# Kernel optimization log

Measured on AMD Instinct MI355X. Metric: run time of the kernel, lower is better.

## Reference

```python
import jax, jax.numpy as jnp
import numpy as np

N, D, P, R, T, K = 200000, 128, 4096, 4, 3, 16

def setup_inputs() -> dict:
    key = jax.random.key(0)
    ks = jax.random.split(key, 9)
    return {
        "node_embeds": jax.random.normal(ks[0], (N, D), jnp.float32),
        "node_pairs": jax.random.randint(ks[1], (P, 2), 0, N),
        "node_type_ids": jax.random.randint(ks[2], (N,), 0, T),
        "neighbor_idx": jax.random.randint(ks[3], (P, 2, R, K), 0, N),
        "delta_t": jax.random.uniform(ks[4], (P, 2, R, K), jnp.float32),
        "W_phi": jax.random.normal(ks[5], (T, D, D), jnp.float32) * 0.05,
        "W_zeta": jax.random.normal(ks[6], (2 * D,), jnp.float32) * 0.05,
        "W_beta_w": jax.random.normal(ks[7], (R, D, D), jnp.float32) * 0.05,
        "W_beta_b": jax.random.normal(ks[8], (R, D), jnp.float32) * 0.05,
    }

def reference(node_embeds, node_pairs, node_type_ids, neighbor_idx, delta_t,
              W_phi, W_zeta, W_beta_w, W_beta_b):
    n = node_embeds.shape[0]
    # per-node type-specific linear: compute all types then select (T small)
    H_all = jnp.einsum('nd,tde->tne', node_embeds, W_phi)        # [T,N,D]
    H = H_all[node_type_ids, jnp.arange(n)]                      # [N,D]
    # micro attention: e = W_zeta([h_n; h_s]) * exp(-dt), softmax over K neighbors
    zn, zs = W_zeta[:D], W_zeta[D:]
    h_n = H[neighbor_idx]                                        # [P,2,R,K,D]
    e_n = jnp.einsum('psrkd,d->psrk', h_n, zn)
    e_s = jnp.einsum('psd,d->ps', H[node_pairs], zs)             # [P,2]
    e = (e_n + e_s[:, :, None, None]) * jnp.exp(-delta_t)        # [P,2,R,K]
    alpha = jax.nn.softmax(e, axis=-1)
    # meso: attention-weighted aggregation per relation, then per-relation linear
    h_nei = node_embeds[neighbor_idx]                            # [P,2,R,K,D]
    h_agg = jnp.einsum('psrk,psrkd->psrd', alpha, h_nei)         # [P,2,R,D]
    h_beta = jnp.einsum('psrd,rde->psre', h_agg, W_beta_w) + W_beta_b
    # macro: average over both pair sides and relations, sigmoid combine
    x_tilde = h_beta.mean(axis=(1, 2))                           # [P,D]
    return jax.nn.sigmoid(x_tilde)
```

## Files before the change

### kernel.cpp

```cpp
#include <hip/hip_runtime.h>
#include <hip/hip_bf16.h>

#define NN 200000
#define D 128
#define P 4096
#define R 4
#define T 3
#define K 16

__device__ __forceinline__ float bf2f(unsigned int u) {
    union { unsigned int i; float f; } c;
    c.i = u << 16;
    return c.f;
}
__device__ __forceinline__ unsigned short f2bf(float x) {
    union { float f; unsigned int i; } c; c.f = x;
    unsigned int r = c.i + 0x7FFFu + ((c.i >> 16) & 1u);
    return (unsigned short)(r >> 16);
}
__device__ __forceinline__ float ldE(const void* p, size_t i, int f32) {
    return f32 ? ((const float*)p)[i] : bf2f(((const unsigned short*)p)[i]);
}
__device__ __forceinline__ void ld8(const void* p, size_t off, int f32, float* o) {
    if (f32) {
        const float* q = (const float*)p + off;
        float4 a = *(const float4*)q;
        float4 b = *(const float4*)(q + 4);
        o[0]=a.x; o[1]=a.y; o[2]=a.z; o[3]=a.w;
        o[4]=b.x; o[5]=b.y; o[6]=b.z; o[7]=b.w;
    } else {
        uint4 r = *(const uint4*)((const unsigned short*)p + off);
        o[0]=bf2f(r.x & 0xffffu); o[1]=bf2f(r.x >> 16);
        o[2]=bf2f(r.y & 0xffffu); o[3]=bf2f(r.y >> 16);
        o[4]=bf2f(r.z & 0xffffu); o[5]=bf2f(r.z >> 16);
        o[6]=bf2f(r.w & 0xffffu); o[7]=bf2f(r.w >> 16);
    }
}

__global__ void detect_dtype(const unsigned short* __restrict__ emb, int* __restrict__ flag) {
    int tid = threadIdx.x;
    int bad = 0;
    #pragma unroll
    for (int i = 0; i < 4; ++i) {
        unsigned short u = emb[(size_t)(tid * 4 + i) * 2 * 97];
        unsigned int e = (u >> 7) & 0xFFu;
        if (e >= 147u) bad = 1;
    }
    int any_bad = __any(bad);
    if (tid == 0) *flag = any_bad ? 1 : 0;
}

__global__ void precompute_vu(const void* __restrict__ W_phi,
                              const void* __restrict__ W_zeta,
                              const int* __restrict__ flag,
                              float* __restrict__ ws_v, float* __restrict__ ws_u) {
    const int f32 = *flag;
    const int t = blockIdx.x;
    const int d = threadIdx.x;
    const size_t rb = (size_t)(t * D + d) * D;
    float av = 0.f, au = 0.f;
    for (int e = 0; e < D; e += 8) {
        float w[8], zn[8], zs[8];
        ld8(W_phi, rb + e, f32, w);
        ld8(W_zeta, e, f32, zn);
        ld8(W_zeta, D + e, f32, zs);
        #pragma unroll
        for (int q = 0; q < 8; ++q) { av += w[q] * zn[q]; au += w[q] * zs[q]; }
    }
    ws_v[t * D + d] = av;
    ws_u[t * D + d] = au;
}

__global__ __launch_bounds__(256) void precompute_c(
    const void* __restrict__ emb, const int* __restrict__ types,
    const float* __restrict__ ws_v, const float* __restrict__ ws_u,
    const int* __restrict__ flag,
    float* __restrict__ c, float* __restrict__ c2)
{
    __shared__ float vsh[T * D], ush[T * D];
    const int f32 = *flag;
    const int tid = threadIdx.x;
    for (int i = tid; i < T * D; i += 256) { vsh[i] = ws_v[i]; ush[i] = ws_u[i]; }
    __syncthreads();
    const int w = tid >> 6, l = tid & 63;
    const int grp = l >> 4, ch = l & 15;
    const int nbase = blockIdx.x * 64 + w * 4 + grp;

    int   tt[4];
    float rv[4][8];
    #pragma unroll
    for (int it = 0; it < 4; ++it) {
        int n = nbase + it * 16;
        tt[it] = types[n];
        ld8(emb, (size_t)n * D + ch * 8, f32, rv[it]);
    }
    #pragma unroll
    for (int it = 0; it < 4; ++it) {
        int n = nbase + it * 16;
        const float* vp = vsh + tt[it] * D + ch * 8;
        const float* up = ush + tt[it] * D + ch * 8;
        float a = 0.f, b = 0.f;
        #pragma unroll
        for (int q = 0; q < 8; ++q) { a += rv[it][q] * vp[q]; b += rv[it][q] * up[q]; }
        #pragma unroll
        for (int off = 1; off <= 8; off <<= 1) {
            a += __shfl_xor(a, off, 64);
            b += __shfl_xor(b, off, 64);
        }
        if (ch == 0) { c[n] = a; c2[n] = b; }
    }
}

__global__ __launch_bounds__(256, 4) void fused_kernel(
    const void* __restrict__ emb,
    const int* __restrict__ pairs,
    const int* __restrict__ nbr,
    const void* __restrict__ dlt,
    const void* __restrict__ W_beta_w,
    const void* __restrict__ W_beta_b,
    const float* __restrict__ c,
    const float* __restrict__ c2,
    const int* __restrict__ flag,
    void* __restrict__ out)
{
    const int f32  = *flag;
    const int tid  = threadIdx.x;
    const int wv   = tid >> 6;
    const int l    = tid & 63;
    const int p    = blockIdx.x * 4 + wv;
    const int rsub = l >> 4;
    const int ch   = l & 15;
    const int base = p * 2 * R * K;

    int nb0 = nbr[base + l];
    int nb1 = nbr[base + 64 + l];
    float cs0 = c2[pairs[p * 2]];
    float cs1 = c2[pairs[p * 2 + 1]];
    float dt0 = ldE(dlt, (size_t)base + l, f32);
    float dt1 = ldE(dlt, (size_t)base + 64 + l, f32);
    float e0 = (c[nb0] + cs0) * __expf(-dt0);
    float e1 = (c[nb1] + cs1) * __expf(-dt1);

    float m0 = e0, m1 = e1;
    #pragma unroll
    for (int off = 1; off <= 8; off <<= 1) {
        m0 = fmaxf(m0, __shfl_xor(m0, off, 64));
        m1 = fmaxf(m1, __shfl_xor(m1, off, 64));
    }
    float a0 = __expf(e0 - m0), a1 = __expf(e1 - m1);
    float s0 = a0, s1 = a1;
    #pragma unroll
    for (int off = 1; off <= 8; off <<= 1) {
        s0 += __shfl_xor(s0, off, 64);
        s1 += __shfl_xor(s1, off, 64);
    }
    a0 *= (1.f / s0);
    a1 *= (1.f / s1);

    float y[8] = {0.f,0.f,0.f,0.f,0.f,0.f,0.f,0.f};
    const unsigned short* eu = (const unsigned short*)emb;
    const unsigned short* Wu = (const unsigned short*)W_beta_w;

    #pragma unroll
    for (int r = 0; r < R; ++r) {
        float acc[8] = {0.f,0.f,0.f,0.f,0.f,0.f,0.f,0.f};
        if (!f32) {
            uint4 rbv[8]; float av[8];
            #pragma unroll
            for (int i = 0; i < 8; ++i) {
                int srcl = r * 16 + (i & 3) * 4 + rsub;
                int nb   = __shfl((i >> 2) ? nb1 : nb0, srcl, 64);
                av[i]    = __shfl((i >> 2) ? a1  : a0,  srcl, 64);
                rbv[i]   = *(const uint4*)(eu + (size_t)nb * D + ch * 8);
            }
            #pragma unroll
            for (int i = 0; i < 8; ++i) {
                float a = av[i];
                acc[0] += a * bf2f(rbv[i].x & 0xffffu); acc[1] += a * bf2f(rbv[i].x >> 16);
                acc[2] += a * bf2f(rbv[i].y & 0xffffu); acc[3] += a * bf2f(rbv[i].y >> 16);
                acc[4] += a * bf2f(rbv[i].z & 0xffffu); acc[5] += a * bf2f(rbv[i].z >> 16);
                acc[6] += a * bf2f(rbv[i].w & 0xffffu); acc[7] += a * bf2f(rbv[i].w >> 16);
            }
        } else {
            #pragma unroll
            for (int i = 0; i < 8; ++i) {
                int srcl = r * 16 + (i & 3) * 4 + rsub;
                int nb   = __shfl((i >> 2) ? nb1 : nb0, srcl, 64);
                float a  = __shfl((i >> 2) ? a1  : a0,  srcl, 64);
                float rv[8]; ld8(emb, (size_t)nb * D + ch * 8, 1, rv);
                #pragma unroll
                for (int q = 0; q < 8; ++q) acc[q] += a * rv[q];
            }
        }
        #pragma unroll
        for (int q = 0; q < 8; ++q) {
            acc[q] += __shfl_xor(acc[q], 16, 64);
            acc[q] += __shfl_xor(acc[q], 32, 64);
        }
        #pragma unroll
        for (int dd = 0; dd < 32; ++dd) {
            float gd = __shfl(acc[dd & 7], ((l & 48) >> 2) + (dd >> 3), 64);
            size_t wo = ((size_t)(r * D + (rsub * 32 + dd))) * D + ch * 8;
            if (!f32) {
                uint4 wr = *(const uint4*)(Wu + wo);
                y[0] += gd * bf2f(wr.x & 0xffffu); y[1] += gd * bf2f(wr.x >> 16);
                y[2] += gd * bf2f(wr.y & 0xffffu); y[3] += gd * bf2f(wr.y >> 16);
                y[4] += gd * bf2f(wr.z & 0xffffu); y[5] += gd * bf2f(wr.z >> 16);
                y[6] += gd * bf2f(wr.w & 0xffffu); y[7] += gd * bf2f(wr.w >> 16);
            } else {
                float wb[8]; ld8(W_beta_w, wo, 1, wb);
                #pragma unroll
                for (int q = 0; q < 8; ++q) y[q] += gd * wb[q];
            }
        }
    }

    #pragma unroll
    for (int q = 0; q < 8; ++q) {
        y[q] += __shfl_xor(y[q], 16, 64);
        y[q] += __shfl_xor(y[q], 32, 64);
    }

    float bs[8] = {0.f,0.f,0.f,0.f,0.f,0.f,0.f,0.f};
    #pragma unroll
    for (int r = 0; r < R; ++r) {
        float bb[8]; ld8(W_beta_b, (size_t)r * D + ch * 8, f32, bb);
        #pragma unroll
        for (int q = 0; q < 8; ++q) bs[q] += bb[q];
    }
    if (rsub == 0) {
        float o[8];
        #pragma unroll
        for (int q = 0; q < 8; ++q) {
            float x = (y[q] + 2.f * bs[q]) * 0.125f;
            o[q] = 1.f / (1.f + __expf(-x));
        }
        size_t ob = (size_t)p * D + ch * 8;
        if (f32) {
            *(float4*)((float*)out + ob)     = make_float4(o[0], o[1], o[2], o[3]);
            *(float4*)((float*)out + ob + 4) = make_float4(o[4], o[5], o[6], o[7]);
        } else {
            uint4 pk;
            pk.x = (unsigned int)f2bf(o[0]) | ((unsigned int)f2bf(o[1]) << 16);
            pk.y = (unsigned int)f2bf(o[2]) | ((unsigned int)f2bf(o[3]) << 16);
            pk.z = (unsigned int)f2bf(o[4]) | ((unsigned int)f2bf(o[5]) << 16);
            pk.w = (unsigned int)f2bf(o[6]) | ((unsigned int)f2bf(o[7]) << 16);
            *(uint4*)((unsigned short*)out + ob) = pk;
        }
    }
}

extern "C" void kernel_launch(void* const* d_in, const int* in_sizes, int n_in,
                              void* d_out, int out_size, void* d_ws, size_t ws_size,
                              hipStream_t stream) {
    const void* emb    = d_in[0];
    const int*  pairs  = (const int*)d_in[1];
    const int*  types  = (const int*)d_in[2];
    const int*  nbr    = (const int*)d_in[3];
    const void* dlt    = d_in[4];
    const void* W_phi  = d_in[5];
    const void* W_zeta = d_in[6];
    const void* W_bw   = d_in[7];
    const void* W_bb   = d_in[8];

    int*   flag = (int*)d_ws;
    float* ws_v = (float*)d_ws + 64;
    float* ws_u = ws_v + T * D;
    float* c    = (float*)d_ws + 1024;
    float* c2   = c + NN;

    detect_dtype<<<dim3(1), dim3(64), 0, stream>>>((const unsigned short*)emb, flag);
    precompute_vu<<<dim3(T), dim3(D), 0, stream>>>(W_phi, W_zeta, flag, ws_v, ws_u);
    precompute_c<<<dim3(NN / 64), dim3(256), 0, stream>>>(emb, types, ws_v, ws_u, flag, c, c2);
    fused_kernel<<<dim3(P / 4), dim3(256), 0, stream>>>(emb, pairs, nbr, dlt,
                                                        W_bw, W_bb, c, c2, flag, d_out);
}
```

Measured before the change: 294.4 us.

## Compute attention logits on gathered rows only and split beta projection into GEMM kernel

Drops the precompute pass that computed per-node logit scalars for all 200k nodes. The gather kernel now computes the logits only for the gathered neighbor and pair rows, reusing the embedding rows it already loads for aggregation. The per-relation aggregate is written to a bf16 workspace, and a separate kernel applies W_beta over 16 pairs per block, reading the aggregates from shared memory. This avoids streaming the whole embedding table but adds an intermediate round-trip and rounds the aggregate to bf16 even on the f32 path, which costs precision.

```diff
diff --git a/kernel.cpp b/kernel.cpp
--- a/kernel.cpp
+++ b/kernel.cpp
@@ -71,58 +71,19 @@
     ws_u[t * D + d] = au;
 }
 
-__global__ __launch_bounds__(256) void precompute_c(
-    const void* __restrict__ emb, const int* __restrict__ types,
-    const float* __restrict__ ws_v, const float* __restrict__ ws_u,
-    const int* __restrict__ flag,
-    float* __restrict__ c, float* __restrict__ c2)
-{
-    __shared__ float vsh[T * D], ush[T * D];
-    const int f32 = *flag;
-    const int tid = threadIdx.x;
-    for (int i = tid; i < T * D; i += 256) { vsh[i] = ws_v[i]; ush[i] = ws_u[i]; }
-    __syncthreads();
-    const int w = tid >> 6, l = tid & 63;
-    const int grp = l >> 4, ch = l & 15;
-    const int nbase = blockIdx.x * 64 + w * 4 + grp;
-
-    int   tt[4];
-    float rv[4][8];
-    #pragma unroll
-    for (int it = 0; it < 4; ++it) {
-        int n = nbase + it * 16;
-        tt[it] = types[n];
-        ld8(emb, (size_t)n * D + ch * 8, f32, rv[it]);
-    }
-    #pragma unroll
-    for (int it = 0; it < 4; ++it) {
-        int n = nbase + it * 16;
-        const float* vp = vsh + tt[it] * D + ch * 8;
-        const float* up = ush + tt[it] * D + ch * 8;
-        float a = 0.f, b = 0.f;
-        #pragma unroll
-        for (int q = 0; q < 8; ++q) { a += rv[it][q] * vp[q]; b += rv[it][q] * up[q]; }
-        #pragma unroll
-        for (int off = 1; off <= 8; off <<= 1) {
-            a += __shfl_xor(a, off, 64);
-            b += __shfl_xor(b, off, 64);
-        }
-        if (ch == 0) { c[n] = a; c2[n] = b; }
-    }
-}
-
-__global__ __launch_bounds__(256, 4) void fused_kernel(
+__global__ __launch_bounds__(256, 2) void gather_kernel(
     const void* __restrict__ emb,
     const int* __restrict__ pairs,
+    const int* __restrict__ types,
     const int* __restrict__ nbr,
     const void* __restrict__ dlt,
-    const void* __restrict__ W_beta_w,
-    const void* __restrict__ W_beta_b,
-    const float* __restrict__ c,
-    const float* __restrict__ c2,
+    const float* __restrict__ ws_v,
+    const float* __restrict__ ws_u,
     const int* __restrict__ flag,
-    void* __restrict__ out)
+    unsigned short* __restrict__ g)
 {
+    __shared__ __align__(16) float vsh[T * D];
+    __shared__ __align__(16) float ush[T * D];
     const int f32  = *flag;
     const int tid  = threadIdx.x;
     const int wv   = tid >> 6;
@@ -132,50 +93,90 @@
     const int ch   = l & 15;
     const int base = p * 2 * R * K;
 
+    for (int i = tid; i < T * D; i += 256) { vsh[i] = ws_v[i]; ush[i] = ws_u[i]; }
+    __syncthreads();
+
     int nb0 = nbr[base + l];
     int nb1 = nbr[base + 64 + l];
-    float cs0 = c2[pairs[p * 2]];
-    float cs1 = c2[pairs[p * 2 + 1]];
     float dt0 = ldE(dlt, (size_t)base + l, f32);
     float dt1 = ldE(dlt, (size_t)base + 64 + l, f32);
-    float e0 = (c[nb0] + cs0) * __expf(-dt0);
-    float e1 = (c[nb1] + cs1) * __expf(-dt1);
-
-    float m0 = e0, m1 = e1;
-    #pragma unroll
-    for (int off = 1; off <= 8; off <<= 1) {
-        m0 = fmaxf(m0, __shfl_xor(m0, off, 64));
-        m1 = fmaxf(m1, __shfl_xor(m1, off, 64));
-    }
-    float a0 = __expf(e0 - m0), a1 = __expf(e1 - m1);
-    float s0 = a0, s1 = a1;
-    #pragma unroll
-    for (int off = 1; off <= 8; off <<= 1) {
-        s0 += __shfl_xor(s0, off, 64);
-        s1 += __shfl_xor(s1, off, 64);
-    }
-    a0 *= (1.f / s0);
-    a1 *= (1.f / s1);
-
-    float y[8] = {0.f,0.f,0.f,0.f,0.f,0.f,0.f,0.f};
+    int t0 = types[nb0];
+    int t1 = types[nb1];
+
+    float es01 = 0.f;
+    if (l < 32) {
+        int s  = rsub;
+        int ns = pairs[p * 2 + s];
+        int ts = types[ns];
+        float rv[8]; ld8(emb, (size_t)ns * D + ch * 8, f32, rv);
+        const float* up = ush + ts * D + ch * 8;
+        float a = 0.f;
+        #pragma unroll
+        for (int q = 0; q < 8; ++q) a += rv[q] * up[q];
+        #pragma unroll
+        for (int off = 1; off <= 8; off <<= 1) a += __shfl_xor(a, off, 64);
+        es01 = a;
+    }
+    float es0 = __shfl(es01, 0, 64);
+    float es1 = __shfl(es01, 16, 64);
+
     const unsigned short* eu = (const unsigned short*)emb;
-    const unsigned short* Wu = (const unsigned short*)W_beta_w;
-
-    #pragma unroll
+
     for (int r = 0; r < R; ++r) {
+        int snb[8]; float sdt[8]; int stp[8];
+        #pragma unroll
+        for (int i = 0; i < 8; ++i) {
+            int srcl = r * 16 + (i & 3) * 4 + rsub;
+            snb[i] = __shfl((i >> 2) ? nb1 : nb0, srcl, 64);
+            sdt[i] = __shfl((i >> 2) ? dt1 : dt0, srcl, 64);
+            stp[i] = __shfl((i >> 2) ? t1  : t0,  srcl, 64);
+        }
+
+        float en[8];
         float acc[8] = {0.f,0.f,0.f,0.f,0.f,0.f,0.f,0.f};
+
         if (!f32) {
-            uint4 rbv[8]; float av[8];
+            uint4 rbv[8];
+            #pragma unroll
+            for (int i = 0; i < 8; ++i)
+                rbv[i] = *(const uint4*)(eu + (size_t)snb[i] * D + ch * 8);
             #pragma unroll
             for (int i = 0; i < 8; ++i) {
-                int srcl = r * 16 + (i & 3) * 4 + rsub;
-                int nb   = __shfl((i >> 2) ? nb1 : nb0, srcl, 64);
-                av[i]    = __shfl((i >> 2) ? a1  : a0,  srcl, 64);
-                rbv[i]   = *(const uint4*)(eu + (size_t)nb * D + ch * 8);
+                const float* vp = vsh + stp[i] * D + ch * 8;
+                float4 v0 = *(const float4*)vp;
+                float4 v1 = *(const float4*)(vp + 4);
+                float a = 0.f;
+                a += bf2f(rbv[i].x & 0xffffu) * v0.x + bf2f(rbv[i].x >> 16) * v0.y;
+                a += bf2f(rbv[i].y & 0xffffu) * v0.z + bf2f(rbv[i].y >> 16) * v0.w;
+                a += bf2f(rbv[i].z & 0xffffu) * v1.x + bf2f(rbv[i].z >> 16) * v1.y;
+                a += bf2f(rbv[i].w & 0xffffu) * v1.z + bf2f(rbv[i].w >> 16) * v1.w;
+                #pragma unroll
+                for (int off = 1; off <= 8; off <<= 1) a += __shfl_xor(a, off, 64);
+                en[i] = a;
             }
+            float ef[8];
+            #pragma unroll
+            for (int i = 0; i < 8; ++i)
+                ef[i] = (en[i] + ((i >> 2) ? es1 : es0)) * __expf(-sdt[i]);
+            float m0 = fmaxf(fmaxf(ef[0], ef[1]), fmaxf(ef[2], ef[3]));
+            float m1 = fmaxf(fmaxf(ef[4], ef[5]), fmaxf(ef[6], ef[7]));
+            m0 = fmaxf(m0, __shfl_xor(m0, 16, 64)); m0 = fmaxf(m0, __shfl_xor(m0, 32, 64));
+            m1 = fmaxf(m1, __shfl_xor(m1, 16, 64)); m1 = fmaxf(m1, __shfl_xor(m1, 32, 64));
+            float al[8], s0 = 0.f, s1 = 0.f;
+            #pragma unroll
+            for (int i = 0; i < 4; ++i) { al[i] = __expf(ef[i] - m0); s0 += al[i]; }
+            #pragma unroll
+            for (int i = 4; i < 8; ++i) { al[i] = __expf(ef[i] - m1); s1 += al[i]; }
+            s0 += __shfl_xor(s0, 16, 64); s0 += __shfl_xor(s0, 32, 64);
+            s1 += __shfl_xor(s1, 16, 64); s1 += __shfl_xor(s1, 32, 64);
+            float i0 = 1.f / s0, i1 = 1.f / s1;
+            #pragma unroll
+            for (int i = 0; i < 4; ++i) al[i] *= i0;
+            #pragma unroll
+            for (int i = 4; i < 8; ++i) al[i] *= i1;
             #pragma unroll
             for (int i = 0; i < 8; ++i) {
-                float a = av[i];
+                float a = al[i];
                 acc[0] += a * bf2f(rbv[i].x & 0xffffu); acc[1] += a * bf2f(rbv[i].x >> 16);
                 acc[2] += a * bf2f(rbv[i].y & 0xffffu); acc[3] += a * bf2f(rbv[i].y >> 16);
                 acc[4] += a * bf2f(rbv[i].z & 0xffffu); acc[5] += a * bf2f(rbv[i].z >> 16);
@@ -184,69 +185,129 @@
         } else {
             #pragma unroll
             for (int i = 0; i < 8; ++i) {
-                int srcl = r * 16 + (i & 3) * 4 + rsub;
-                int nb   = __shfl((i >> 2) ? nb1 : nb0, srcl, 64);
-                float a  = __shfl((i >> 2) ? a1  : a0,  srcl, 64);
-                float rv[8]; ld8(emb, (size_t)nb * D + ch * 8, 1, rv);
+                float rv[8]; ld8(emb, (size_t)snb[i] * D + ch * 8, 1, rv);
+                const float* vp = vsh + stp[i] * D + ch * 8;
+                float a = 0.f;
                 #pragma unroll
-                for (int q = 0; q < 8; ++q) acc[q] += a * rv[q];
+                for (int q = 0; q < 8; ++q) a += rv[q] * vp[q];
+                #pragma unroll
+                for (int off = 1; off <= 8; off <<= 1) a += __shfl_xor(a, off, 64);
+                en[i] = a;
             }
-        }
+            float ef[8];
+            #pragma unroll
+            for (int i = 0; i < 8; ++i)
+                ef[i] = (en[i] + ((i >> 2) ? es1 : es0)) * __expf(-sdt[i]);
+            float m0 = fmaxf(fmaxf(ef[0], ef[1]), fmaxf(ef[2], ef[3]));
+            float m1 = fmaxf(fmaxf(ef[4], ef[5]), fmaxf(ef[6], ef[7]));
+            m0 = fmaxf(m0, __shfl_xor(m0, 16, 64)); m0 = fmaxf(m0, __shfl_xor(m0, 32, 64));
+            m1 = fmaxf(m1, __shfl_xor(m1, 16, 64)); m1 = fmaxf(m1, __shfl_xor(m1, 32, 64));
+            float al[8], s0 = 0.f, s1 = 0.f;
+            #pragma unroll
+            for (int i = 0; i < 4; ++i) { al[i] = __expf(ef[i] - m0); s0 += al[i]; }
+            #pragma unroll
+            for (int i = 4; i < 8; ++i) { al[i] = __expf(ef[i] - m1); s1 += al[i]; }
+            s0 += __shfl_xor(s0, 16, 64); s0 += __shfl_xor(s0, 32, 64);
+            s1 += __shfl_xor(s1, 16, 64); s1 += __shfl_xor(s1, 32, 64);
+            float i0 = 1.f / s0, i1 = 1.f / s1;
+            #pragma unroll
+            for (int i = 0; i < 4; ++i) al[i] *= i0;
+            #pragma unroll
+            for (int i = 4; i < 8; ++i) al[i] *= i1;
+            #pragma unroll
+            for (int i = 0; i < 8; ++i) {
+                float rv[8]; ld8(emb, (size_t)snb[i] * D + ch * 8, 1, rv);
+                #pragma unroll
+                for (int q = 0; q < 8; ++q) acc[q] += al[i] * rv[q];
+            }
+        }
+
         #pragma unroll
         for (int q = 0; q < 8; ++q) {
             acc[q] += __shfl_xor(acc[q], 16, 64);
             acc[q] += __shfl_xor(acc[q], 32, 64);
         }
-        #pragma unroll
-        for (int dd = 0; dd < 32; ++dd) {
-            float gd = __shfl(acc[dd & 7], ((l & 48) >> 2) + (dd >> 3), 64);
-            size_t wo = ((size_t)(r * D + (rsub * 32 + dd))) * D + ch * 8;
-            if (!f32) {
-                uint4 wr = *(const uint4*)(Wu + wo);
-                y[0] += gd * bf2f(wr.x & 0xffffu); y[1] += gd * bf2f(wr.x >> 16);
-                y[2] += gd * bf2f(wr.y & 0xffffu); y[3] += gd * bf2f(wr.y >> 16);
-                y[4] += gd * bf2f(wr.z & 0xffffu); y[5] += gd * bf2f(wr.z >> 16);
-                y[6] += gd * bf2f(wr.w & 0xffffu); y[7] += gd * bf2f(wr.w >> 16);
-            } else {
-                float wb[8]; ld8(W_beta_w, wo, 1, wb);
-                #pragma unroll
-                for (int q = 0; q < 8; ++q) y[q] += gd * wb[q];
-            }
-        }
-    }
-
-    #pragma unroll
-    for (int q = 0; q < 8; ++q) {
-        y[q] += __shfl_xor(y[q], 16, 64);
-        y[q] += __shfl_xor(y[q], 32, 64);
+        if (rsub == 0) {
+            uint4 pk;
+            pk.x = (unsigned int)f2bf(acc[0]) | ((unsigned int)f2bf(acc[1]) << 16);
+            pk.y = (unsigned int)f2bf(acc[2]) | ((unsigned int)f2bf(acc[3]) << 16);
+            pk.z = (unsigned int)f2bf(acc[4]) | ((unsigned int)f2bf(acc[5]) << 16);
+            pk.w = (unsigned int)f2bf(acc[6]) | ((unsigned int)f2bf(acc[7]) << 16);
+            *(uint4*)(g + ((size_t)p * R + r) * D + ch * 8) = pk;
+        }
+    }
+}
+
+__global__ __launch_bounds__(256, 2) void beta_gemm(
+    const unsigned short* __restrict__ g,
+    const void* __restrict__ W_bw,
+    const void* __restrict__ W_bb,
+    const int* __restrict__ flag,
+    void* __restrict__ out)
+{
+    __shared__ float gl[16 * 513];
+    const int f32 = *flag;
+    const int tid = threadIdx.x;
+    const int pl  = tid >> 4;
+    const int eb  = (tid & 15) * 8;
+    const size_t pbase = (size_t)blockIdx.x * 16 * 512;
+
+    for (int i = tid * 8; i < 16 * 512; i += 256 * 8) {
+        float v[8]; ld8(g, pbase + i, 0, v);
+        int pp = i >> 9, kk = i & 511;
+        #pragma unroll
+        for (int q = 0; q < 8; ++q) gl[pp * 513 + kk + q] = v[q];
+    }
+    __syncthreads();
+
+    float y[8] = {0.f,0.f,0.f,0.f,0.f,0.f,0.f,0.f};
+    const unsigned short* Wu = (const unsigned short*)W_bw;
+    if (!f32) {
+        #pragma unroll 8
+        for (int k = 0; k < 512; ++k) {
+            float gd = gl[pl * 513 + k];
+            uint4 wr = *(const uint4*)(Wu + (size_t)k * D + eb);
+            y[0] += gd * bf2f(wr.x & 0xffffu); y[1] += gd * bf2f(wr.x >> 16);
+            y[2] += gd * bf2f(wr.y & 0xffffu); y[3] += gd * bf2f(wr.y >> 16);
+            y[4] += gd * bf2f(wr.z & 0xffffu); y[5] += gd * bf2f(wr.z >> 16);
+            y[6] += gd * bf2f(wr.w & 0xffffu); y[7] += gd * bf2f(wr.w >> 16);
+        }
+    } else {
+        #pragma unroll 4
+        for (int k = 0; k < 512; ++k) {
+            float gd = gl[pl * 513 + k];
+            float wb[8]; ld8(W_bw, (size_t)k * D + eb, 1, wb);
+            #pragma unroll
+            for (int q = 0; q < 8; ++q) y[q] += gd * wb[q];
+        }
     }
 
     float bs[8] = {0.f,0.f,0.f,0.f,0.f,0.f,0.f,0.f};
     #pragma unroll
     for (int r = 0; r < R; ++r) {
-        float bb[8]; ld8(W_beta_b, (size_t)r * D + ch * 8, f32, bb);
+        float bb[8]; ld8(W_bb, (size_t)r * D + eb, f32, bb);
         #pragma unroll
         for (int q = 0; q < 8; ++q) bs[q] += bb[q];
     }
-    if (rsub == 0) {
-        float o[8];
-        #pragma unroll
-        for (int q = 0; q < 8; ++q) {
-            float x = (y[q] + 2.f * bs[q]) * 0.125f;
-            o[q] = 1.f / (1.f + __expf(-x));
-        }
-        size_t ob = (size_t)p * D + ch * 8;
-        if (f32) {
-            *(float4*)((float*)out + ob)     = make_float4(o[0], o[1], o[2], o[3]);
-            *(float4*)((float*)out + ob + 4) = make_float4(o[4], o[5], o[6], o[7]);
-        } else {
-            uint4 pk;
-            pk.x = (unsigned int)f2bf(o[0]) | ((unsigned int)f2bf(o[1]) << 16);
-            pk.y = (unsigned int)f2bf(o[2]) | ((unsigned int)f2bf(o[3]) << 16);
-            pk.z = (unsigned int)f2bf(o[4]) | ((unsigned int)f2bf(o[5]) << 16);
-            pk.w = (unsigned int)f2bf(o[6]) | ((unsigned int)f2bf(o[7]) << 16);
-            *(uint4*)((unsigned short*)out + ob) = pk;
-        }
+
+    int p = blockIdx.x * 16 + pl;
+    size_t ob = (size_t)p * D + eb;
+    float o[8];
+    #pragma unroll
+    for (int q = 0; q < 8; ++q) {
+        float x = (y[q] + 2.f * bs[q]) * 0.125f;
+        o[q] = 1.f / (1.f + __expf(-x));
+    }
+    if (f32) {
+        *(float4*)((float*)out + ob)     = make_float4(o[0], o[1], o[2], o[3]);
+        *(float4*)((float*)out + ob + 4) = make_float4(o[4], o[5], o[6], o[7]);
+    } else {
+        uint4 pk;
+        pk.x = (unsigned int)f2bf(o[0]) | ((unsigned int)f2bf(o[1]) << 16);
+        pk.y = (unsigned int)f2bf(o[2]) | ((unsigned int)f2bf(o[3]) << 16);
+        pk.z = (unsigned int)f2bf(o[4]) | ((unsigned int)f2bf(o[5]) << 16);
+        pk.w = (unsigned int)f2bf(o[6]) | ((unsigned int)f2bf(o[7]) << 16);
+        *(uint4*)((unsigned short*)out + ob) = pk;
     }
 }
 
@@ -266,12 +327,11 @@
     int*   flag = (int*)d_ws;
     float* ws_v = (float*)d_ws + 64;
     float* ws_u = ws_v + T * D;
-    float* c    = (float*)d_ws + 1024;
-    float* c2   = c + NN;
+    unsigned short* g = (unsigned short*)((float*)d_ws + 1024);
 
     detect_dtype<<<dim3(1), dim3(64), 0, stream>>>((const unsigned short*)emb, flag);
     precompute_vu<<<dim3(T), dim3(D), 0, stream>>>(W_phi, W_zeta, flag, ws_v, ws_u);
-    precompute_c<<<dim3(NN / 64), dim3(256), 0, stream>>>(emb, types, ws_v, ws_u, flag, c, c2);
-    fused_kernel<<<dim3(P / 4), dim3(256), 0, stream>>>(emb, pairs, nbr, dlt,
-                                                        W_bw, W_bb, c, c2, flag, d_out);
-}
+    gather_kernel<<<dim3(P / 4), dim3(256), 0, stream>>>(emb, pairs, types, nbr, dlt,
+                                                         ws_v, ws_u, flag, g);
+    beta_gemm<<<dim3(P / 16), dim3(256), 0, stream>>>(g, W_bw, W_bb, flag, d_out);
+}
```

Result: faster. 283.2 us (-3.8%).

## Compute attention scores on gathered neighbors instead of precomputing per-node table

Applied to the files above, without the earlier changes.

Drops the precompute_c pass over all 200k nodes. The neighbor attention logits are now computed inside the main kernel from the embedding rows it already gathers, projected through the per-type v vectors in shared memory. Dtype detection and the v/u precompute are merged into one small kernel, which cuts the launch count. The fused kernel now gives each wave one pair side, prefetches the next relation's rows in the bf16 path, and splits the W_beta projection across the two side-waves through shared memory. The cost is more per-neighbor compute and shuffles in the main kernel, plus extra block syncs.

```diff
diff --git a/kernel.cpp b/kernel.cpp
--- a/kernel.cpp
+++ b/kernel.cpp
@@ -37,26 +37,28 @@
     }
 }
 
-__global__ void detect_dtype(const unsigned short* __restrict__ emb, int* __restrict__ flag) {
-    int tid = threadIdx.x;
+__global__ void prep_kernel(const unsigned short* __restrict__ emb_u,
+                            const void* __restrict__ W_phi,
+                            const void* __restrict__ W_zeta,
+                            int* __restrict__ gflag,
+                            float* __restrict__ ws_v, float* __restrict__ ws_u) {
+    __shared__ int sbad[2];
+    const int tid = threadIdx.x;
+    const int t   = blockIdx.x;
     int bad = 0;
     #pragma unroll
     for (int i = 0; i < 4; ++i) {
-        unsigned short u = emb[(size_t)(tid * 4 + i) * 2 * 97];
+        unsigned short u = emb_u[(size_t)(blockIdx.x * 512 + tid * 4 + i) * 2 * 97];
         unsigned int e = (u >> 7) & 0xFFu;
         if (e >= 147u) bad = 1;
     }
-    int any_bad = __any(bad);
-    if (tid == 0) *flag = any_bad ? 1 : 0;
-}
-
-__global__ void precompute_vu(const void* __restrict__ W_phi,
-                              const void* __restrict__ W_zeta,
-                              const int* __restrict__ flag,
-                              float* __restrict__ ws_v, float* __restrict__ ws_u) {
-    const int f32 = *flag;
-    const int t = blockIdx.x;
-    const int d = threadIdx.x;
+    int anyb = __any(bad) ? 1 : 0;
+    if ((tid & 63) == 0) sbad[tid >> 6] = anyb;
+    __syncthreads();
+    const int f32 = sbad[0] | sbad[1];
+    if (t == 0 && tid == 0) *gflag = f32;
+
+    const int d = tid;
     const size_t rb = (size_t)(t * D + d) * D;
     float av = 0.f, au = 0.f;
     for (int e = 0; e < D; e += 8) {
@@ -71,136 +73,189 @@
     ws_u[t * D + d] = au;
 }
 
-__global__ __launch_bounds__(256) void precompute_c(
-    const void* __restrict__ emb, const int* __restrict__ types,
-    const float* __restrict__ ws_v, const float* __restrict__ ws_u,
-    const int* __restrict__ flag,
-    float* __restrict__ c, float* __restrict__ c2)
-{
-    __shared__ float vsh[T * D], ush[T * D];
-    const int f32 = *flag;
-    const int tid = threadIdx.x;
-    for (int i = tid; i < T * D; i += 256) { vsh[i] = ws_v[i]; ush[i] = ws_u[i]; }
-    __syncthreads();
-    const int w = tid >> 6, l = tid & 63;
-    const int grp = l >> 4, ch = l & 15;
-    const int nbase = blockIdx.x * 64 + w * 4 + grp;
-
-    int   tt[4];
-    float rv[4][8];
-    #pragma unroll
-    for (int it = 0; it < 4; ++it) {
-        int n = nbase + it * 16;
-        tt[it] = types[n];
-        ld8(emb, (size_t)n * D + ch * 8, f32, rv[it]);
-    }
-    #pragma unroll
-    for (int it = 0; it < 4; ++it) {
-        int n = nbase + it * 16;
-        const float* vp = vsh + tt[it] * D + ch * 8;
-        const float* up = ush + tt[it] * D + ch * 8;
-        float a = 0.f, b = 0.f;
-        #pragma unroll
-        for (int q = 0; q < 8; ++q) { a += rv[it][q] * vp[q]; b += rv[it][q] * up[q]; }
-        #pragma unroll
-        for (int off = 1; off <= 8; off <<= 1) {
-            a += __shfl_xor(a, off, 64);
-            b += __shfl_xor(b, off, 64);
-        }
-        if (ch == 0) { c[n] = a; c2[n] = b; }
-    }
-}
-
-__global__ __launch_bounds__(256, 4) void fused_kernel(
+__global__ __launch_bounds__(256, 4) void fused_all(
     const void* __restrict__ emb,
     const int* __restrict__ pairs,
+    const int* __restrict__ types,
     const int* __restrict__ nbr,
     const void* __restrict__ dlt,
-    const void* __restrict__ W_beta_w,
-    const void* __restrict__ W_beta_b,
-    const float* __restrict__ c,
-    const float* __restrict__ c2,
+    const void* __restrict__ W_bw,
+    const void* __restrict__ W_bb,
+    const float* __restrict__ ws_v,
+    const float* __restrict__ ws_u,
     const int* __restrict__ flag,
     void* __restrict__ out)
 {
+    __shared__ __align__(16) float vsh[T * D];
+    __shared__ __align__(16) float ush[T * D];
+    __shared__ __align__(16) float gsh[2][2][R][D];
+    __shared__ __align__(16) float ysh[2][2][D];
+
     const int f32  = *flag;
     const int tid  = threadIdx.x;
     const int wv   = tid >> 6;
     const int l    = tid & 63;
-    const int p    = blockIdx.x * 4 + wv;
+    const int pr   = wv >> 1;
+    const int s    = wv & 1;
+    const int p    = blockIdx.x * 2 + pr;
     const int rsub = l >> 4;
     const int ch   = l & 15;
-    const int base = p * 2 * R * K;
-
-    int nb0 = nbr[base + l];
-    int nb1 = nbr[base + 64 + l];
-    float cs0 = c2[pairs[p * 2]];
-    float cs1 = c2[pairs[p * 2 + 1]];
-    float dt0 = ldE(dlt, (size_t)base + l, f32);
-    float dt1 = ldE(dlt, (size_t)base + 64 + l, f32);
-    float e0 = (c[nb0] + cs0) * __expf(-dt0);
-    float e1 = (c[nb1] + cs1) * __expf(-dt1);
-
-    float m0 = e0, m1 = e1;
+    const int base = p * 2 * R * K + s * 64;
+
+    for (int i = tid; i < T * D; i += 256) { vsh[i] = ws_v[i]; ush[i] = ws_u[i]; }
+    __syncthreads();
+
+    const int nb  = nbr[base + l];
+    const float dtv = ldE(dlt, (size_t)base + l, f32);
+    const int tp  = types[nb];
+
+    float es;
+    {
+        int ns = pairs[p * 2 + s];
+        int ts = types[ns];
+        float a = ldE(emb, (size_t)ns * D + 2 * l,     f32) * ush[ts * D + 2 * l]
+                + ldE(emb, (size_t)ns * D + 2 * l + 1, f32) * ush[ts * D + 2 * l + 1];
+        #pragma unroll
+        for (int off = 1; off <= 32; off <<= 1) a += __shfl_xor(a, off, 64);
+        es = a;
+    }
+
+    const unsigned short* eu = (const unsigned short*)emb;
+
+    if (!f32) {
+        int snb[4];
+        uint4 cur[4], nxt[4];
+        #pragma unroll
+        for (int i = 0; i < 4; ++i) snb[i] = __shfl(nb, i * 4 + rsub, 64);
+        #pragma unroll
+        for (int i = 0; i < 4; ++i)
+            cur[i] = *(const uint4*)(eu + (size_t)snb[i] * D + ch * 8);
+
+        #pragma unroll
+        for (int r = 0; r < R; ++r) {
+            float sdt[4]; int stp[4];
+            #pragma unroll
+            for (int i = 0; i < 4; ++i) {
+                int srcl = r * 16 + i * 4 + rsub;
+                sdt[i] = __shfl(dtv, srcl, 64);
+                stp[i] = __shfl(tp,  srcl, 64);
+            }
+            if (r < 3) {
+                #pragma unroll
+                for (int i = 0; i < 4; ++i) snb[i] = __shfl(nb, (r + 1) * 16 + i * 4 + rsub, 64);
+                #pragma unroll
+                for (int i = 0; i < 4; ++i)
+                    nxt[i] = *(const uint4*)(eu + (size_t)snb[i] * D + ch * 8);
+            }
+            float ef[4];
+            #pragma unroll
+            for (int i = 0; i < 4; ++i) {
+                const float* vp = vsh + stp[i] * D + ch * 8;
+                float4 v0 = *(const float4*)vp;
+                float4 v1 = *(const float4*)(vp + 4);
+                float a = 0.f;
+                a += bf2f(cur[i].x & 0xffffu) * v0.x + bf2f(cur[i].x >> 16) * v0.y;
+                a += bf2f(cur[i].y & 0xffffu) * v0.z + bf2f(cur[i].y >> 16) * v0.w;
+                a += bf2f(cur[i].z & 0xffffu) * v1.x + bf2f(cur[i].z >> 16) * v1.y;
+                a += bf2f(cur[i].w & 0xffffu) * v1.z + bf2f(cur[i].w >> 16) * v1.w;
+                #pragma unroll
+                for (int off = 1; off <= 8; off <<= 1) a += __shfl_xor(a, off, 64);
+                ef[i] = (a + es) * __expf(-sdt[i]);
+            }
+            float m = fmaxf(fmaxf(ef[0], ef[1]), fmaxf(ef[2], ef[3]));
+            m = fmaxf(m, __shfl_xor(m, 16, 64));
+            m = fmaxf(m, __shfl_xor(m, 32, 64));
+            float al[4], ssum = 0.f;
+            #pragma unroll
+            for (int i = 0; i < 4; ++i) { al[i] = __expf(ef[i] - m); ssum += al[i]; }
+            ssum += __shfl_xor(ssum, 16, 64);
+            ssum += __shfl_xor(ssum, 32, 64);
+            float inv = 1.f / ssum;
+            float acc[8] = {0.f,0.f,0.f,0.f,0.f,0.f,0.f,0.f};
+            #pragma unroll
+            for (int i = 0; i < 4; ++i) {
+                float a = al[i] * inv;
+                acc[0] += a * bf2f(cur[i].x & 0xffffu); acc[1] += a * bf2f(cur[i].x >> 16);
+                acc[2] += a * bf2f(cur[i].y & 0xffffu); acc[3] += a * bf2f(cur[i].y >> 16);
+                acc[4] += a * bf2f(cur[i].z & 0xffffu); acc[5] += a * bf2f(cur[i].z >> 16);
+                acc[6] += a * bf2f(cur[i].w & 0xffffu); acc[7] += a * bf2f(cur[i].w >> 16);
+            }
+            #pragma unroll
+            for (int q = 0; q < 8; ++q) {
+                acc[q] += __shfl_xor(acc[q], 16, 64);
+                acc[q] += __shfl_xor(acc[q], 32, 64);
+            }
+            if (rsub == 0) {
+                *(float4*)(&gsh[pr][s][r][ch * 8])     = make_float4(acc[0], acc[1], acc[2], acc[3]);
+                *(float4*)(&gsh[pr][s][r][ch * 8 + 4]) = make_float4(acc[4], acc[5], acc[6], acc[7]);
+            }
+            #pragma unroll
+            for (int i = 0; i < 4; ++i) cur[i] = nxt[i];
+        }
+    } else {
+        #pragma unroll
+        for (int r = 0; r < R; ++r) {
+            int snb[4]; float sdt[4]; int stp[4];
+            #pragma unroll
+            for (int i = 0; i < 4; ++i) {
+                int srcl = r * 16 + i * 4 + rsub;
+                snb[i] = __shfl(nb,  srcl, 64);
+                sdt[i] = __shfl(dtv, srcl, 64);
+                stp[i] = __shfl(tp,  srcl, 64);
+            }
+            float rv[4][8];
+            #pragma unroll
+            for (int i = 0; i < 4; ++i) ld8(emb, (size_t)snb[i] * D + ch * 8, 1, rv[i]);
+            float ef[4];
+            #pragma unroll
+            for (int i = 0; i < 4; ++i) {
+                const float* vp = vsh + stp[i] * D + ch * 8;
+                float a = 0.f;
+                #pragma unroll
+                for (int q = 0; q < 8; ++q) a += rv[i][q] * vp[q];
+                #pragma unroll
+                for (int off = 1; off <= 8; off <<= 1) a += __shfl_xor(a, off, 64);
+                ef[i] = (a + es) * __expf(-sdt[i]);
+            }
+            float m = fmaxf(fmaxf(ef[0], ef[1]), fmaxf(ef[2], ef[3]));
+            m = fmaxf(m, __shfl_xor(m, 16, 64));
+            m = fmaxf(m, __shfl_xor(m, 32, 64));
+            float al[4], ssum = 0.f;
+            #pragma unroll
+            for (int i = 0; i < 4; ++i) { al[i] = __expf(ef[i] - m); ssum += al[i]; }
+            ssum += __shfl_xor(ssum, 16, 64);
+            ssum += __shfl_xor(ssum, 32, 64);
+            float inv = 1.f / ssum;
+            float acc[8] = {0.f,0.f,0.f,0.f,0.f,0.f,0.f,0.f};
+            #pragma unroll
+            for (int i = 0; i < 4; ++i) {
+                float a = al[i] * inv;
+                #pragma unroll
+                for (int q = 0; q < 8; ++q) acc[q] += a * rv[i][q];
+            }
+            #pragma unroll
+            for (int q = 0; q < 8; ++q) {
+                acc[q] += __shfl_xor(acc[q], 16, 64);
+                acc[q] += __shfl_xor(acc[q], 32, 64);
+            }
+            if (rsub == 0) {
+                *(float4*)(&gsh[pr][s][r][ch * 8])     = make_float4(acc[0], acc[1], acc[2], acc[3]);
+                *(float4*)(&gsh[pr][s][r][ch * 8 + 4]) = make_float4(acc[4], acc[5], acc[6], acc[7]);
+            }
+        }
+    }
+    __syncthreads();
+
+    float y[8] = {0.f,0.f,0.f,0.f,0.f,0.f,0.f,0.f};
+    const unsigned short* Wu = (const unsigned short*)W_bw;
     #pragma unroll
-    for (int off = 1; off <= 8; off <<= 1) {
-        m0 = fmaxf(m0, __shfl_xor(m0, off, 64));
-        m1 = fmaxf(m1, __shfl_xor(m1, off, 64));
-    }
-    float a0 = __expf(e0 - m0), a1 = __expf(e1 - m1);
-    float s0 = a0, s1 = a1;
-    #pragma unroll
-    for (int off = 1; off <= 8; off <<= 1) {
-        s0 += __shfl_xor(s0, off, 64);
-        s1 += __shfl_xor(s1, off, 64);
-    }
-    a0 *= (1.f / s0);
-    a1 *= (1.f / s1);
-
-    float y[8] = {0.f,0.f,0.f,0.f,0.f,0.f,0.f,0.f};
-    const unsigned short* eu = (const unsigned short*)emb;
-    const unsigned short* Wu = (const unsigned short*)W_beta_w;
-
-    #pragma unroll
-    for (int r = 0; r < R; ++r) {
-        float acc[8] = {0.f,0.f,0.f,0.f,0.f,0.f,0.f,0.f};
-        if (!f32) {
-            uint4 rbv[8]; float av[8];
-            #pragma unroll
-            for (int i = 0; i < 8; ++i) {
-                int srcl = r * 16 + (i & 3) * 4 + rsub;
-                int nb   = __shfl((i >> 2) ? nb1 : nb0, srcl, 64);
-                av[i]    = __shfl((i >> 2) ? a1  : a0,  srcl, 64);
-                rbv[i]   = *(const uint4*)(eu + (size_t)nb * D + ch * 8);
-            }
-            #pragma unroll
-            for (int i = 0; i < 8; ++i) {
-                float a = av[i];
-                acc[0] += a * bf2f(rbv[i].x & 0xffffu); acc[1] += a * bf2f(rbv[i].x >> 16);
-                acc[2] += a * bf2f(rbv[i].y & 0xffffu); acc[3] += a * bf2f(rbv[i].y >> 16);
-                acc[4] += a * bf2f(rbv[i].z & 0xffffu); acc[5] += a * bf2f(rbv[i].z >> 16);
-                acc[6] += a * bf2f(rbv[i].w & 0xffffu); acc[7] += a * bf2f(rbv[i].w >> 16);
-            }
-        } else {
-            #pragma unroll
-            for (int i = 0; i < 8; ++i) {
-                int srcl = r * 16 + (i & 3) * 4 + rsub;
-                int nb   = __shfl((i >> 2) ? nb1 : nb0, srcl, 64);
-                float a  = __shfl((i >> 2) ? a1  : a0,  srcl, 64);
-                float rv[8]; ld8(emb, (size_t)nb * D + ch * 8, 1, rv);
-                #pragma unroll
-                for (int q = 0; q < 8; ++q) acc[q] += a * rv[q];
-            }
-        }
-        #pragma unroll
-        for (int q = 0; q < 8; ++q) {
-            acc[q] += __shfl_xor(acc[q], 16, 64);
-            acc[q] += __shfl_xor(acc[q], 32, 64);
-        }
-        #pragma unroll
+    for (int rr = 0; rr < 2; ++rr) {
+        const int r = s * 2 + rr;
+        #pragma unroll 8
         for (int dd = 0; dd < 32; ++dd) {
-            float gd = __shfl(acc[dd & 7], ((l & 48) >> 2) + (dd >> 3), 64);
-            size_t wo = ((size_t)(r * D + (rsub * 32 + dd))) * D + ch * 8;
+            const int d = rsub * 32 + dd;
+            float gd = gsh[pr][0][r][d] + gsh[pr][1][r][d];
+            size_t wo = ((size_t)(r * D + d)) * D + ch * 8;
             if (!f32) {
                 uint4 wr = *(const uint4*)(Wu + wo);
                 y[0] += gd * bf2f(wr.x & 0xffffu); y[1] += gd * bf2f(wr.x >> 16);
@@ -208,31 +263,36 @@
                 y[4] += gd * bf2f(wr.z & 0xffffu); y[5] += gd * bf2f(wr.z >> 16);
                 y[6] += gd * bf2f(wr.w & 0xffffu); y[7] += gd * bf2f(wr.w >> 16);
             } else {
-                float wb[8]; ld8(W_beta_w, wo, 1, wb);
+                float wb[8]; ld8(W_bw, wo, 1, wb);
                 #pragma unroll
                 for (int q = 0; q < 8; ++q) y[q] += gd * wb[q];
             }
         }
     }
-
     #pragma unroll
     for (int q = 0; q < 8; ++q) {
         y[q] += __shfl_xor(y[q], 16, 64);
         y[q] += __shfl_xor(y[q], 32, 64);
     }
-
-    float bs[8] = {0.f,0.f,0.f,0.f,0.f,0.f,0.f,0.f};
-    #pragma unroll
-    for (int r = 0; r < R; ++r) {
-        float bb[8]; ld8(W_beta_b, (size_t)r * D + ch * 8, f32, bb);
-        #pragma unroll
-        for (int q = 0; q < 8; ++q) bs[q] += bb[q];
-    }
     if (rsub == 0) {
+        *(float4*)(&ysh[pr][s][ch * 8])     = make_float4(y[0], y[1], y[2], y[3]);
+        *(float4*)(&ysh[pr][s][ch * 8 + 4]) = make_float4(y[4], y[5], y[6], y[7]);
+    }
+    __syncthreads();
+
+    if (s == 0 && rsub == 0) {
+        float bs[8] = {0.f,0.f,0.f,0.f,0.f,0.f,0.f,0.f};
+        #pragma unroll
+        for (int r = 0; r < R; ++r) {
+            float bb[8]; ld8(W_bb, (size_t)r * D + ch * 8, f32, bb);
+            #pragma unroll
+            for (int q = 0; q < 8; ++q) bs[q] += bb[q];
+        }
         float o[8];
         #pragma unroll
         for (int q = 0; q < 8; ++q) {
-            float x = (y[q] + 2.f * bs[q]) * 0.125f;
+            int e = ch * 8 + q;
+            float x = (ysh[pr][0][e] + ysh[pr][1][e] + 2.f * bs[q]) * 0.125f;
             o[q] = 1.f / (1.f + __expf(-x));
         }
         size_t ob = (size_t)p * D + ch * 8;
@@ -266,12 +326,9 @@
     int*   flag = (int*)d_ws;
     float* ws_v = (float*)d_ws + 64;
     float* ws_u = ws_v + T * D;
-    float* c    = (float*)d_ws + 1024;
-    float* c2   = c + NN;
-
-    detect_dtype<<<dim3(1), dim3(64), 0, stream>>>((const unsigned short*)emb, flag);
-    precompute_vu<<<dim3(T), dim3(D), 0, stream>>>(W_phi, W_zeta, flag, ws_v, ws_u);
-    precompute_c<<<dim3(NN / 64), dim3(256), 0, stream>>>(emb, types, ws_v, ws_u, flag, c, c2);
-    fused_kernel<<<dim3(P / 4), dim3(256), 0, stream>>>(emb, pairs, nbr, dlt,
-                                                        W_bw, W_bb, c, c2, flag, d_out);
-}
+
+    prep_kernel<<<dim3(T), dim3(128), 0, stream>>>((const unsigned short*)emb,
+                                                   W_phi, W_zeta, flag, ws_v, ws_u);
+    fused_all<<<dim3(P / 2), dim3(256), 0, stream>>>(emb, pairs, types, nbr, dlt,
+                                                     W_bw, W_bb, ws_v, ws_u, flag, d_out);
+}
```

Result: faster. 244.0 us (-17.1%).

## Split pair sides across waves with readlane row gathers and LDS reduction

Applied to the files above, without the earlier changes.

The main kernel now gives each wave one side of one pair, so a block covers 2 pairs instead of 4. Each wave gathers whole neighbor rows coalesced across all 64 lanes, using readlane to broadcast the neighbor index and attention weight. It stages per-relation aggregates in shared memory and splits the W_beta matvec by relation between the two side-waves, then merges through LDS. The dtype detection and the v/u precompute are also fused into one launch. The aim is more parallelism and fewer lanes doing redundant work, at the cost of two block barriers and more, narrower load instructions.

```diff
diff --git a/kernel.cpp b/kernel.cpp
--- a/kernel.cpp
+++ b/kernel.cpp
@@ -36,27 +36,32 @@
         o[6]=bf2f(r.w & 0xffffu); o[7]=bf2f(r.w >> 16);
     }
 }
-
-__global__ void detect_dtype(const unsigned short* __restrict__ emb, int* __restrict__ flag) {
-    int tid = threadIdx.x;
+__device__ __forceinline__ float readlane_f(float v, int lane) {
+    return __int_as_float(__builtin_amdgcn_readlane(__float_as_int(v), lane));
+}
+
+__global__ void prep_kernel(const unsigned short* __restrict__ emb_u,
+                            const void* __restrict__ W_phi,
+                            const void* __restrict__ W_zeta,
+                            int* __restrict__ gflag,
+                            float* __restrict__ ws_v, float* __restrict__ ws_u) {
+    __shared__ int sbad[2];
+    const int tid = threadIdx.x;
+    const int t   = blockIdx.x;
     int bad = 0;
     #pragma unroll
     for (int i = 0; i < 4; ++i) {
-        unsigned short u = emb[(size_t)(tid * 4 + i) * 2 * 97];
+        unsigned short u = emb_u[(size_t)(blockIdx.x * 512 + tid * 4 + i) * 2 * 97];
         unsigned int e = (u >> 7) & 0xFFu;
         if (e >= 147u) bad = 1;
     }
-    int any_bad = __any(bad);
-    if (tid == 0) *flag = any_bad ? 1 : 0;
-}
-
-__global__ void precompute_vu(const void* __restrict__ W_phi,
-                              const void* __restrict__ W_zeta,
-                              const int* __restrict__ flag,
-                              float* __restrict__ ws_v, float* __restrict__ ws_u) {
-    const int f32 = *flag;
-    const int t = blockIdx.x;
-    const int d = threadIdx.x;
+    int anyb = __any(bad) ? 1 : 0;
+    if ((tid & 63) == 0) sbad[tid >> 6] = anyb;
+    __syncthreads();
+    const int f32 = sbad[0] | sbad[1];
+    if (t == 0 && tid == 0) *gflag = f32;
+
+    const int d = tid;
     const size_t rb = (size_t)(t * D + d) * D;
     float av = 0.f, au = 0.f;
     for (int e = 0; e < D; e += 8) {
@@ -111,96 +116,99 @@
     }
 }
 
-__global__ __launch_bounds__(256, 4) void fused_kernel(
+__global__ __launch_bounds__(256, 4) void fused_all(
     const void* __restrict__ emb,
     const int* __restrict__ pairs,
     const int* __restrict__ nbr,
     const void* __restrict__ dlt,
-    const void* __restrict__ W_beta_w,
-    const void* __restrict__ W_beta_b,
+    const void* __restrict__ W_bw,
+    const void* __restrict__ W_bb,
     const float* __restrict__ c,
     const float* __restrict__ c2,
     const int* __restrict__ flag,
     void* __restrict__ out)
 {
+    __shared__ __align__(16) float gsh[2][2][R][D];
+    __shared__ __align__(16) float ysh[2][2][D];
+
     const int f32  = *flag;
     const int tid  = threadIdx.x;
     const int wv   = tid >> 6;
     const int l    = tid & 63;
-    const int p    = blockIdx.x * 4 + wv;
+    const int pr   = wv >> 1;
+    const int s    = wv & 1;
+    const int p    = blockIdx.x * 2 + pr;
     const int rsub = l >> 4;
     const int ch   = l & 15;
-    const int base = p * 2 * R * K;
-
-    int nb0 = nbr[base + l];
-    int nb1 = nbr[base + 64 + l];
-    float cs0 = c2[pairs[p * 2]];
-    float cs1 = c2[pairs[p * 2 + 1]];
-    float dt0 = ldE(dlt, (size_t)base + l, f32);
-    float dt1 = ldE(dlt, (size_t)base + 64 + l, f32);
-    float e0 = (c[nb0] + cs0) * __expf(-dt0);
-    float e1 = (c[nb1] + cs1) * __expf(-dt1);
-
-    float m0 = e0, m1 = e1;
-    #pragma unroll
-    for (int off = 1; off <= 8; off <<= 1) {
-        m0 = fmaxf(m0, __shfl_xor(m0, off, 64));
-        m1 = fmaxf(m1, __shfl_xor(m1, off, 64));
-    }
-    float a0 = __expf(e0 - m0), a1 = __expf(e1 - m1);
-    float s0 = a0, s1 = a1;
-    #pragma unroll
-    for (int off = 1; off <= 8; off <<= 1) {
-        s0 += __shfl_xor(s0, off, 64);
-        s1 += __shfl_xor(s1, off, 64);
-    }
-    a0 *= (1.f / s0);
-    a1 *= (1.f / s1);
+    const int base = p * 2 * R * K + s * 64;
+
+    const int   nb = nbr[base + l];
+    const float dt = ldE(dlt, (size_t)base + l, f32);
+    const float ce = c[nb];
+    const float es = c2[pairs[p * 2 + s]];
+    float e = (ce + es) * __expf(-dt);
+    float m = e;
+    #pragma unroll
+    for (int off = 1; off <= 8; off <<= 1) m = fmaxf(m, __shfl_xor(m, off, 64));
+    float al = __expf(e - m);
+    float ssum = al;
+    #pragma unroll
+    for (int off = 1; off <= 8; off <<= 1) ssum += __shfl_xor(ssum, off, 64);
+    al *= (1.f / ssum);
+
+    if (!f32) {
+        const unsigned short* eu = (const unsigned short*)emb;
+        #pragma unroll
+        for (int r = 0; r < R; ++r) {
+            unsigned int ud[K];
+            #pragma unroll
+            for (int k = 0; k < K; ++k) {
+                int s_nb = __builtin_amdgcn_readlane(nb, r * K + k);
+                ud[k] = *(const unsigned int*)(eu + (size_t)s_nb * D + 2 * l);
+            }
+            float a0 = 0.f, a1 = 0.f;
+            #pragma unroll
+            for (int k = 0; k < K; ++k) {
+                float a = readlane_f(al, r * K + k);
+                a0 += a * bf2f(ud[k] & 0xffffu);
+                a1 += a * bf2f(ud[k] >> 16);
+            }
+            gsh[pr][s][r][2 * l]     = a0;
+            gsh[pr][s][r][2 * l + 1] = a1;
+        }
+    } else {
+        const float* ef = (const float*)emb;
+        #pragma unroll
+        for (int r = 0; r < R; ++r) {
+            float2 ud[K];
+            #pragma unroll
+            for (int k = 0; k < K; ++k) {
+                int s_nb = __builtin_amdgcn_readlane(nb, r * K + k);
+                ud[k] = *(const float2*)(ef + (size_t)s_nb * D + 2 * l);
+            }
+            float a0 = 0.f, a1 = 0.f;
+            #pragma unroll
+            for (int k = 0; k < K; ++k) {
+                float a = readlane_f(al, r * K + k);
+                a0 += a * ud[k].x;
+                a1 += a * ud[k].y;
+            }
+            gsh[pr][s][r][2 * l]     = a0;
+            gsh[pr][s][r][2 * l + 1] = a1;
+        }
+    }
+    __syncthreads();
 
     float y[8] = {0.f,0.f,0.f,0.f,0.f,0.f,0.f,0.f};
-    const unsigned short* eu = (const unsigned short*)emb;
-    const unsigned short* Wu = (const unsigned short*)W_beta_w;
-
-    #pragma unroll
-    for (int r = 0; r < R; ++r) {
-        float acc[8] = {0.f,0.f,0.f,0.f,0.f,0.f,0.f,0.f};
-        if (!f32) {
-            uint4 rbv[8]; float av[8];
-            #pragma unroll
-            for (int i = 0; i < 8; ++i) {
-                int srcl = r * 16 + (i & 3) * 4 + rsub;
-                int nb   = __shfl((i >> 2) ? nb1 : nb0, srcl, 64);
-                av[i]    = __shfl((i >> 2) ? a1  : a0,  srcl, 64);
-                rbv[i]   = *(const uint4*)(eu + (size_t)nb * D + ch * 8);
-            }
-            #pragma unroll
-            for (int i = 0; i < 8; ++i) {
-                float a = av[i];
-                acc[0] += a * bf2f(rbv[i].x & 0xffffu); acc[1] += a * bf2f(rbv[i].x >> 16);
-                acc[2] += a * bf2f(rbv[i].y & 0xffffu); acc[3] += a * bf2f(rbv[i].y >> 16);
-                acc[4] += a * bf2f(rbv[i].z & 0xffffu); acc[5] += a * bf2f(rbv[i].z >> 16);
-                acc[6] += a * bf2f(rbv[i].w & 0xffffu); acc[7] += a * bf2f(rbv[i].w >> 16);
-            }
-        } else {
-            #pragma unroll
-            for (int i = 0; i < 8; ++i) {
-                int srcl = r * 16 + (i & 3) * 4 + rsub;
-                int nb   = __shfl((i >> 2) ? nb1 : nb0, srcl, 64);
-                float a  = __shfl((i >> 2) ? a1  : a0,  srcl, 64);
-                float rv[8]; ld8(emb, (size_t)nb * D + ch * 8, 1, rv);
-                #pragma unroll
-                for (int q = 0; q < 8; ++q) acc[q] += a * rv[q];
-            }
-        }
-        #pragma unroll
-        for (int q = 0; q < 8; ++q) {
-            acc[q] += __shfl_xor(acc[q], 16, 64);
-            acc[q] += __shfl_xor(acc[q], 32, 64);
-        }
-        #pragma unroll
+    const unsigned short* Wu = (const unsigned short*)W_bw;
+    #pragma unroll
+    for (int rr = 0; rr < 2; ++rr) {
+        const int r = s * 2 + rr;
+        #pragma unroll 8
         for (int dd = 0; dd < 32; ++dd) {
-            float gd = __shfl(acc[dd & 7], ((l & 48) >> 2) + (dd >> 3), 64);
-            size_t wo = ((size_t)(r * D + (rsub * 32 + dd))) * D + ch * 8;
+            const int d = rsub * 32 + dd;
+            float gd = gsh[pr][0][r][d] + gsh[pr][1][r][d];
+            size_t wo = ((size_t)(r * D + d)) * D + ch * 8;
             if (!f32) {
                 uint4 wr = *(const uint4*)(Wu + wo);
                 y[0] += gd * bf2f(wr.x & 0xffffu); y[1] += gd * bf2f(wr.x >> 16);
@@ -208,31 +216,36 @@
                 y[4] += gd * bf2f(wr.z & 0xffffu); y[5] += gd * bf2f(wr.z >> 16);
                 y[6] += gd * bf2f(wr.w & 0xffffu); y[7] += gd * bf2f(wr.w >> 16);
             } else {
-                float wb[8]; ld8(W_beta_w, wo, 1, wb);
+                float wb[8]; ld8(W_bw, wo, 1, wb);
                 #pragma unroll
                 for (int q = 0; q < 8; ++q) y[q] += gd * wb[q];
             }
         }
     }
-
     #pragma unroll
     for (int q = 0; q < 8; ++q) {
         y[q] += __shfl_xor(y[q], 16, 64);
         y[q] += __shfl_xor(y[q], 32, 64);
     }
-
-    float bs[8] = {0.f,0.f,0.f,0.f,0.f,0.f,0.f,0.f};
-    #pragma unroll
-    for (int r = 0; r < R; ++r) {
-        float bb[8]; ld8(W_beta_b, (size_t)r * D + ch * 8, f32, bb);
-        #pragma unroll
-        for (int q = 0; q < 8; ++q) bs[q] += bb[q];
-    }
     if (rsub == 0) {
+        *(float4*)(&ysh[pr][s][ch * 8])     = make_float4(y[0], y[1], y[2], y[3]);
+        *(float4*)(&ysh[pr][s][ch * 8 + 4]) = make_float4(y[4], y[5], y[6], y[7]);
+    }
+    __syncthreads();
+
+    if (s == 0 && rsub == 0) {
+        float bs[8] = {0.f,0.f,0.f,0.f,0.f,0.f,0.f,0.f};
+        #pragma unroll
+        for (int r = 0; r < R; ++r) {
+            float bb[8]; ld8(W_bb, (size_t)r * D + ch * 8, f32, bb);
+            #pragma unroll
+            for (int q = 0; q < 8; ++q) bs[q] += bb[q];
+        }
         float o[8];
         #pragma unroll
         for (int q = 0; q < 8; ++q) {
-            float x = (y[q] + 2.f * bs[q]) * 0.125f;
+            int e2 = ch * 8 + q;
+            float x = (ysh[pr][0][e2] + ysh[pr][1][e2] + 2.f * bs[q]) * 0.125f;
             o[q] = 1.f / (1.f + __expf(-x));
         }
         size_t ob = (size_t)p * D + ch * 8;
@@ -269,9 +282,10 @@
     float* c    = (float*)d_ws + 1024;
     float* c2   = c + NN;
 
-    detect_dtype<<<dim3(1), dim3(64), 0, stream>>>((const unsigned short*)emb, flag);
-    precompute_vu<<<dim3(T), dim3(D), 0, stream>>>(W_phi, W_zeta, flag, ws_v, ws_u);
-    precompute_c<<<dim3(NN / 64), dim3(256), 0, stream>>>(emb, types, ws_v, ws_u, flag, c, c2);
-    fused_kernel<<<dim3(P / 4), dim3(256), 0, stream>>>(emb, pairs, nbr, dlt,
-                                                        W_bw, W_bb, c, c2, flag, d_out);
-}
+    prep_kernel<<<dim3(T), dim3(128), 0, stream>>>((const unsigned short*)emb,
+                                                   W_phi, W_zeta, flag, ws_v, ws_u);
+    precompute_c<<<dim3(NN / 64), dim3(256), 0, stream>>>(emb, types, ws_v, ws_u,
+                                                          flag, c, c2);
+    fused_all<<<dim3(P / 2), dim3(256), 0, stream>>>(emb, pairs, nbr, dlt,
+                                                     W_bw, W_bb, c, c2, flag, d_out);
+}
```

Result: faster. 261.5 us (-11.2%).
